# Kernel optimization log

Measured on AMD Instinct MI355X. Metric: run time of the kernel, lower is better.

The kernel has to match this reference:

```python
import jax, jax.numpy as jnp
import numpy as np

INNER_LR = 0.001
INNER_STEPS = 3
EPS = 1e-8


def setup_inputs() -> dict:
    key = jax.random.key(0)
    ks = jax.random.split(key, 9)
    B_, H, K = 16384, 512, 64
    return {
        "R_U": jax.random.normal(ks[0], (B_, H, 3), dtype=jnp.float32),
        "alpha": jax.random.uniform(ks[1], (B_,), dtype=jnp.float32),
        "beta": jax.random.uniform(ks[2], (B_,), dtype=jnp.float32),
        "lambdas": jax.random.uniform(ks[3], (3,), dtype=jnp.float32),
        "B": jax.random.normal(ks[4], (H, K), dtype=jnp.float32),
        "B_dot": jax.random.normal(ks[5], (H, K), dtype=jnp.float32),
        "B_ddot": jax.random.normal(ks[6], (H, K), dtype=jnp.float32),
        "B_dddot": jax.random.normal(ks[7], (H, K), dtype=jnp.float32),
        "B_pinv": jax.random.normal(ks[8], (K, H), dtype=jnp.float32),
    }


def _inner_opt(R_U, alpha, beta, lambdas, B, B_dot, B_ddot, B_dddot, B_pinv):
    l1, l2, l3 = lambdas[0], lambdas[1], lambdas[2]

    def per_sample(r, a, b):
        # r: (H,3); C: (K,3)
        C0 = B_pinv @ r

        def loss_fn(C):
            P = B @ C            # (H,3)
            V = B_dot @ C        # (H,3)
            A = B_ddot @ C       # (H,3)
            J = B_dddot @ C      # (H,3)
            v_norm_raw = jnp.linalg.norm(V, axis=-1)          # (H,) used in power-law loss
            v_norm_eps = v_norm_raw + EPS                      # used in curvature (torch adds eps)
            cross = jnp.cross(V, A)                            # (H,3)
            kappa = jnp.linalg.norm(cross, axis=-1) / (v_norm_eps ** 3 + EPS)
            pos_loss = jnp.sum((P - r) ** 2, axis=-1)          # (H,)
            kappa_safe = jnp.clip(kappa, 1e-4, 1e4)
            log_power = jnp.clip(b * jnp.log(kappa_safe), -10.0, 10.0)
            target = jnp.clip(a * jnp.exp(log_power), 1e-6, 1e6)
            power_law_loss = (v_norm_raw - target) ** 2        # (H,)
            jerk_loss = jnp.sum(J ** 2, axis=-1)               # (H,)
            return jnp.sum(l1 * pos_loss + l2 * power_law_loss + l3 * jerk_loss)

        def step(C, _):
            g = jax.grad(loss_fn)(C)
            return C - INNER_LR * g, None

        C, _ = jax.lax.scan(step, C0, None, length=INNER_STEPS)
        return C

    return jax.vmap(per_sample)(R_U, alpha, beta)  # (batch, K, 3)


def reference(R_U, alpha, beta, lambdas, B, B_dot, B_ddot, B_dddot, B_pinv):
    return _inner_opt(R_U, alpha, beta, lambdas, B, B_dot, B_ddot, B_dddot, B_pinv)
```

## Files before the change

kernel.cpp:

```cpp
#include <hip/hip_runtime.h>
#include <hip/hip_bf16.h>
#include <math.h>

#define EPSF 1e-8f
#define LR   1e-3f

#define HH 512
#define KK 64
#define SS 8
#define PbStr 104
#define GbStr 136
#define SLICE 4096

typedef short    bf16x8 __attribute__((ext_vector_type(8)));
typedef _Float16 f16x8  __attribute__((ext_vector_type(8)));
typedef _Float16 f16x4  __attribute__((ext_vector_type(4)));
typedef float    f32x4  __attribute__((ext_vector_type(4)));

__device__ __forceinline__ unsigned short f2bf(float x) {
  unsigned int u = __float_as_uint(x);
  return (unsigned short)((u + 0x7fffu + ((u >> 16) & 1u)) >> 16);
}
__device__ __forceinline__ float bfhi(float x) {
  return __uint_as_float(((unsigned int)f2bf(x)) << 16);
}
__device__ __forceinline__ unsigned short f2h(float x) {
  _Float16 h = (_Float16)x;
  return *(unsigned short*)&h;
}
__device__ __forceinline__ unsigned int pkbf2(float a, float b) {
  union { __hip_bfloat162 h; unsigned int u; } cv;
  cv.h = __float22bfloat162_rn(make_float2(a, b));
  return cv.u;
}

__device__ __forceinline__ void elemf(
    float P0, float P1, float P2, float V0, float V1, float V2,
    float A0, float A1, float A2, float J0, float J1, float J2,
    float aa, float bb, float r0, float r1, float r2,
    float l1, float l2, float l3,
    float& o0, float& o1, float& o2, float& o3, float& o4, float& o5,
    float& o6, float& o7, float& o8, float& o9, float& o10, float& o11) {
  float v2 = V0*V0 + V1*V1 + V2*V2;
  float v  = __builtin_amdgcn_sqrtf(v2);
  float ve = v + EPSF;
  float cx0 = V1*A2 - V2*A1;
  float cx1 = V2*A0 - V0*A2;
  float cx2 = V0*A1 - V1*A0;
  float nc  = __builtin_amdgcn_sqrtf(cx0*cx0 + cx1*cx1 + cx2*cx2);
  float ve2 = ve*ve;
  float denom = ve2*ve + EPSF;
  float invd  = __builtin_amdgcn_rcpf(denom);
  float kappa = nc * invd;
  float ks  = fminf(fmaxf(kappa, 1e-4f), 1e4f);
  float lpr = bb * __logf(ks);
  float lp  = fminf(fmaxf(lpr, -10.f), 10.f);
  float tr  = aa * __expf(lp);
  float tt  = fminf(fmaxf(tr, 1e-6f), 1e6f);
  float s2  = 2.f*l2*(v - tt);
  float gtr  = (tr > 1e-6f && tr < 1e6f) ? -s2 : 0.f;
  float glpr = (lpr > -10.f && lpr < 10.f) ? gtr*tr : 0.f;
  float gk   = (kappa > 1e-4f && kappa < 1e4f)
                 ? glpr*bb*__builtin_amdgcn_rcpf(ks) : 0.f;
  float gnc  = gk * invd;
  float gden = -gk * kappa * invd;
  float gve  = 3.f * ve2 * gden;
  float gv   = s2 + gve;
  float giv  = gv * __builtin_amdgcn_rcpf(v);
  float gcs  = gnc * __builtin_amdgcn_rcpf(nc);
  float gc0 = gcs*cx0, gc1 = gcs*cx1, gc2 = gcs*cx2;
  o0  = 2.f*l1*(P0 - r0);
  o1  = 2.f*l1*(P1 - r1);
  o2  = 2.f*l1*(P2 - r2);
  o3  = fmaf(giv, V0, A1*gc2 - A2*gc1);
  o4  = fmaf(giv, V1, A2*gc0 - A0*gc2);
  o5  = fmaf(giv, V2, A0*gc1 - A1*gc0);
  o6  = gc1*V2 - gc2*V1;
  o7  = gc2*V0 - gc0*V2;
  o8  = gc0*V1 - gc1*V0;
  o9  = 2.f*l3*J0;
  o10 = 2.f*l3*J1;
  o11 = 2.f*l3*J2;
}

__global__ void prep_kernel(const float* __restrict__ B,
                            const float* __restrict__ Bd,
                            const float* __restrict__ Bdd,
                            const float* __restrict__ Bddd,
                            const float* __restrict__ Bp,
                            unsigned short* __restrict__ ws) {
  int tid = blockIdx.x * 256 + threadIdx.x;
  const float* Ms[4] = {B, Bd, Bdd, Bddd};
  unsigned short bits[2];
  if (tid < 65536) {
    #pragma unroll
    for (int t = 0; t < 2; ++t) {
      unsigned int id = 2u * tid + t;
      int j = id & 7, lane = (id >> 3) & 63;
      int mt = (id >> 9) & 3, ks2 = (id >> 11) & 3;
      int qtr = (id >> 13) & 3, chunk = (id >> 15) & 3;
      int khat = mt * 16 + (lane & 15);
      int kq = ((lane >> 4) << 3) + j;
      int h = chunk * 128 + qtr * 32 + kq;
      bits[t] = f2bf(Ms[ks2][h * 64 + khat]);
    }
    ((unsigned int*)ws)[tid] = ((unsigned int)bits[1] << 16) | bits[0];
  } else if (tid < 131072) {
    int base = tid - 65536;
    #pragma unroll
    for (int t = 0; t < 2; ++t) {
      unsigned int id = 2u * base + t;
      int j = id & 7, lane = (id >> 3) & 63, kap = (id >> 9) & 1;
      int ht = (id >> 10) & 31, z = (id >> 15) & 3;
      int h = ht * 16 + (lane & 15);
      int kk = kap * 32 + ((lane >> 4) << 3) + j;
      bits[t] = f2h(Ms[z][h * 64 + kk]);
    }
    ((unsigned int*)(ws + 131072))[base] = ((unsigned int)bits[1] << 16) | bits[0];
  } else {
    int base = tid - 131072;
    #pragma unroll
    for (int t = 0; t < 2; ++t) {
      unsigned int id = 2u * base + t;
      int j = id & 7, lane = (id >> 3) & 63, hilo = (id >> 9) & 1;
      int mt = (id >> 10) & 3, ks = (id >> 12) & 15;
      int khat = mt * 16 + (lane & 15);
      int Kl = ks * 32 + ((lane >> 4) << 3) + j;
      float val = Bp[khat * 512 + Kl];
      float hi = bfhi(val);
      bits[t] = hilo ? f2bf(val - hi) : f2bf(hi);
    }
    ((unsigned int*)(ws + 262144))[base] = ((unsigned int)bits[1] << 16) | bits[0];
  }
}

__global__ __launch_bounds__(256, 3)
void copt_kernel(const float* __restrict__ R_U,
                 const float* __restrict__ alpha,
                 const float* __restrict__ beta,
                 const float* __restrict__ lambdas,
                 const unsigned short* __restrict__ ws,
                 float* __restrict__ out) {
  __shared__ __align__(16) float Cl[SS][KK][3];
  __shared__ __align__(16) unsigned short Cbf[2 * 1024];
  __shared__ __align__(16) unsigned short pool[4 * SLICE];

  const unsigned short* AFb = ws;
  const unsigned short* AFf = ws + 131072;
  const unsigned short* AFp = ws + 262144;

  const int tid  = threadIdx.x;
  const int lane = tid & 63;
  const int wid  = tid >> 6;
  const int quad = lane >> 4;
  const int c    = lane & 15;

  const float l1 = lambdas[0], l2 = lambdas[1], l3 = lambdas[2];
  const int bg = blockIdx.x * SS;

  ((float4*)Cbf)[tid] = make_float4(0.f, 0.f, 0.f, 0.f);

  #pragma unroll
  for (int sg2 = 0; sg2 < 2; ++sg2) {
    const int colb = sg2 * 12 + 3 * wid;
    const float4* rp = (const float4*)(R_U + (size_t)(bg + wid + sg2 * 4) * (HH * 3));
    #pragma unroll
    for (int i = 0; i < 6; ++i) {
      float4 v = rp[i * 64 + lane];
      int e = (i * 64 + lane) * 4;
      const float* pv = &v.x;
      #pragma unroll
      for (int d = 0; d < 4; ++d) {
        int ee = e + d, h = ee / 3, m = ee - 3 * h;
        pool[(colb + m) * 520 + h] = f2bf(pv[d]);
      }
    }
  }
  __syncthreads();

  {
    f32x4 cacc0 = {0.f, 0.f, 0.f, 0.f};
    f32x4 cacc1 = {0.f, 0.f, 0.f, 0.f};
    const unsigned short* gb0 = &pool[c * 520 + quad * 8];
    const unsigned short* gb1 = &pool[(12 + c) * 520 + quad * 8];
    #pragma unroll 4
    for (int ks = 0; ks < 16; ++ks) {
      const unsigned short* pA = AFp + (size_t)((ks * 4 + wid) * 2) * 512 + lane * 8;
      bf16x8 ah = *(const bf16x8*)pA;
      bf16x8 al = *(const bf16x8*)(pA + 512);
      bf16x8 g0 = *(const bf16x8*)(gb0 + ks * 32);
      bf16x8 g1 = *(const bf16x8*)(gb1 + ks * 32);
      cacc0 = __builtin_amdgcn_mfma_f32_16x16x32_bf16(ah, g0, cacc0, 0, 0, 0);
      cacc0 = __builtin_amdgcn_mfma_f32_16x16x32_bf16(al, g0, cacc0, 0, 0, 0);
      cacc1 = __builtin_amdgcn_mfma_f32_16x16x32_bf16(ah, g1, cacc1, 0, 0, 0);
      cacc1 = __builtin_amdgcn_mfma_f32_16x16x32_bf16(al, g1, cacc1, 0, 0, 0);
    }
    if (c < 12) {
      const int sl = (c * 86) >> 8, m = c - 3 * sl;
      const int kr = wid * 16 + quad * 4;
      #pragma unroll
      for (int r = 0; r < 4; ++r) {
        int k = kr + r;
        float v0 = cacc0[r];
        Cl[sl][k][m] = v0;
        Cbf[(k >> 5) * 512 + (((k >> 3) & 3) * 16 + c) * 8 + (k & 7)] = f2h(v0);
        float v1 = cacc1[r];
        Cl[sl + 4][k][m] = v1;
        Cbf[1024 + (k >> 5) * 512 + (((k >> 3) & 3) * 16 + c) * 8 + (k & 7)] = f2h(v1);
      }
    }
  }
  __syncthreads();

  const int hq = lane & 31;
  const int esb = 4 * (lane >> 5);
  const float ea0 = alpha[bg + esb + 0], ea1 = alpha[bg + esb + 1];
  const float ea2 = alpha[bg + esb + 2], ea3 = alpha[bg + esb + 3];
  const float eb0 = beta[bg + esb + 0],  eb1 = beta[bg + esb + 1];
  const float eb2 = beta[bg + esb + 2],  eb3 = beta[bg + esb + 3];
  const float* er0 = R_U + (size_t)(bg + esb + 0) * (HH * 3);
  const float* er1 = R_U + (size_t)(bg + esb + 1) * (HH * 3);
  const float* er2 = R_U + (size_t)(bg + esb + 2) * (HH * 3);
  const float* er3 = R_U + (size_t)(bg + esb + 3) * (HH * 3);

  unsigned short* Pbh = pool + wid * SLICE;
  unsigned short* Gbu = pool + wid * SLICE;

  const int fs = (c * 86) >> 8, fm = c - 3 * fs;

  for (int it = 0; it < 3; ++it) {
    f32x4 g00 = {0.f,0.f,0.f,0.f}, g01 = {0.f,0.f,0.f,0.f};
    f32x4 g10 = {0.f,0.f,0.f,0.f}, g11 = {0.f,0.f,0.f,0.f};
    f32x4 g20 = {0.f,0.f,0.f,0.f}, g21 = {0.f,0.f,0.f,0.f};
    f32x4 g30 = {0.f,0.f,0.f,0.f}, g31 = {0.f,0.f,0.f,0.f};

    f16x8 cf00 = *(const f16x8*)&Cbf[lane * 8];
    f16x8 cf01 = *(const f16x8*)&Cbf[512 + lane * 8];
    f16x8 cf10 = *(const f16x8*)&Cbf[1024 + lane * 8];
    f16x8 cf11 = *(const f16x8*)&Cbf[1536 + lane * 8];

    for (int q = 0; q < 4; ++q) {
      #pragma unroll
      for (int ht = 0; ht < 2; ++ht) {
        const int htg = wid * 8 + q * 2 + ht;
        #pragma unroll
        for (int z = 0; z < 4; ++z) {
          const unsigned short* pA =
              AFf + (size_t)((z * 32 + htg) * 2) * 512 + lane * 8;
          f16x8 af0 = *(const f16x8*)pA;
          f16x8 af1 = *(const f16x8*)(pA + 512);
          f32x4 d0 = {0.f, 0.f, 0.f, 0.f};
          d0 = __builtin_amdgcn_mfma_f32_16x16x32_f16(af0, cf00, d0, 0, 0, 0);
          d0 = __builtin_amdgcn_mfma_f32_16x16x32_f16(af1, cf01, d0, 0, 0, 0);
          f32x4 d1 = {0.f, 0.f, 0.f, 0.f};
          d1 = __builtin_amdgcn_mfma_f32_16x16x32_f16(af0, cf10, d1, 0, 0, 0);
          d1 = __builtin_amdgcn_mfma_f32_16x16x32_f16(af1, cf11, d1, 0, 0, 0);
          if (c < 12) {
            unsigned short* pb = Pbh + (ht * 16 + quad * 4) * PbStr + z * 3 + fm;
            unsigned short* pp0 = pb + fs * 12;
            pp0[0 * PbStr] = f2h(d0[0]);
            pp0[1 * PbStr] = f2h(d0[1]);
            pp0[2 * PbStr] = f2h(d0[2]);
            pp0[3 * PbStr] = f2h(d0[3]);
            unsigned short* pp1 = pb + (fs + 4) * 12;
            pp1[0 * PbStr] = f2h(d1[0]);
            pp1[1 * PbStr] = f2h(d1[1]);
            pp1[2 * PbStr] = f2h(d1[2]);
            pp1[3 * PbStr] = f2h(d1[3]);
          }
        }
      }

      {
        const unsigned short* p0 = Pbh + hq * PbStr + (esb + 0) * 12;
        const unsigned short* p1 = Pbh + hq * PbStr + (esb + 1) * 12;
        const unsigned short* p2 = Pbh + hq * PbStr + (esb + 2) * 12;
        const unsigned short* p3 = Pbh + hq * PbStr + (esb + 3) * 12;
        f16x4 va0 = *(const f16x4*)(p0);
        f16x4 va1 = *(const f16x4*)(p0 + 4);
        f16x4 va2 = *(const f16x4*)(p0 + 8);
        f16x4 vb0 = *(const f16x4*)(p1);
        f16x4 vb1 = *(const f16x4*)(p1 + 4);
        f16x4 vb2 = *(const f16x4*)(p1 + 8);
        f16x4 vc0 = *(const f16x4*)(p2);
        f16x4 vc1 = *(const f16x4*)(p2 + 4);
        f16x4 vc2 = *(const f16x4*)(p2 + 8);
        f16x4 vd0 = *(const f16x4*)(p3);
        f16x4 vd1 = *(const f16x4*)(p3 + 4);
        f16x4 vd2 = *(const f16x4*)(p3 + 8);
        const int hg = wid * 128 + q * 32 + hq;
        float r00 = er0[(size_t)hg*3], r01 = er0[(size_t)hg*3+1], r02 = er0[(size_t)hg*3+2];
        float r10 = er1[(size_t)hg*3], r11 = er1[(size_t)hg*3+1], r12 = er1[(size_t)hg*3+2];
        float r20 = er2[(size_t)hg*3], r21 = er2[(size_t)hg*3+1], r22 = er2[(size_t)hg*3+2];
        float r30 = er3[(size_t)hg*3], r31 = er3[(size_t)hg*3+1], r32 = er3[(size_t)hg*3+2];

        float gA0,gA1,gA2,gA3,gA4,gA5,gA6,gA7,gA8,gA9,gA10,gA11;
        float gB0,gB1,gB2,gB3,gB4,gB5,gB6,gB7,gB8,gB9,gB10,gB11;
        elemf((float)va0[0],(float)va0[1],(float)va0[2],(float)va0[3],
              (float)va1[0],(float)va1[1],(float)va1[2],(float)va1[3],
              (float)va2[0],(float)va2[1],(float)va2[2],(float)va2[3],
              ea0, eb0, r00, r01, r02, l1, l2, l3,
              gA0,gA1,gA2,gA3,gA4,gA5,gA6,gA7,gA8,gA9,gA10,gA11);
        elemf((float)vb0[0],(float)vb0[1],(float)vb0[2],(float)vb0[3],
              (float)vb1[0],(float)vb1[1],(float)vb1[2],(float)vb1[3],
              (float)vb2[0],(float)vb2[1],(float)vb2[2],(float)vb2[3],
              ea1, eb1, r10, r11, r12, l1, l2, l3,
              gB0,gB1,gB2,gB3,gB4,gB5,gB6,gB7,gB8,gB9,gB10,gB11);

        #define STOREG(zz, mm, GA, GB, E0, E1) { \
          unsigned int pk = pkbf2(GA, GB); \
          Gbu[(3*(esb+E0) + mm) * GbStr + (zz)*32 + hq] = (unsigned short)pk; \
          Gbu[(3*(esb+E1) + mm) * GbStr + (zz)*32 + hq] = (unsigned short)(pk >> 16); }
        STOREG(0, 0, gA0, gB0, 0, 1)  STOREG(0, 1, gA1, gB1, 0, 1)  STOREG(0, 2, gA2, gB2, 0, 1)
        STOREG(1, 0, gA3, gB3, 0, 1)  STOREG(1, 1, gA4, gB4, 0, 1)  STOREG(1, 2, gA5, gB5, 0, 1)
        STOREG(2, 0, gA6, gB6, 0, 1)  STOREG(2, 1, gA7, gB7, 0, 1)  STOREG(2, 2, gA8, gB8, 0, 1)
        STOREG(3, 0, gA9, gB9, 0, 1)  STOREG(3, 1, gA10, gB10, 0, 1) STOREG(3, 2, gA11, gB11, 0, 1)

        elemf((float)vc0[0],(float)vc0[1],(float)vc0[2],(float)vc0[3],
              (float)vc1[0],(float)vc1[1],(float)vc1[2],(float)vc1[3],
              (float)vc2[0],(float)vc2[1],(float)vc2[2],(float)vc2[3],
              ea2, eb2, r20, r21, r22, l1, l2, l3,
              gA0,gA1,gA2,gA3,gA4,gA5,gA6,gA7,gA8,gA9,gA10,gA11);
        elemf((float)vd0[0],(float)vd0[1],(float)vd0[2],(float)vd0[3],
              (float)vd1[0],(float)vd1[1],(float)vd1[2],(float)vd1[3],
              (float)vd2[0],(float)vd2[1],(float)vd2[2],(float)vd2[3],
              ea3, eb3, r30, r31, r32, l1, l2, l3,
              gB0,gB1,gB2,gB3,gB4,gB5,gB6,gB7,gB8,gB9,gB10,gB11);
        STOREG(0, 0, gA0, gB0, 2, 3)  STOREG(0, 1, gA1, gB1, 2, 3)  STOREG(0, 2, gA2, gB2, 2, 3)
        STOREG(1, 0, gA3, gB3, 2, 3)  STOREG(1, 1, gA4, gB4, 2, 3)  STOREG(1, 2, gA5, gB5, 2, 3)
        STOREG(2, 0, gA6, gB6, 2, 3)  STOREG(2, 1, gA7, gB7, 2, 3)  STOREG(2, 2, gA8, gB8, 2, 3)
        STOREG(3, 0, gA9, gB9, 2, 3)  STOREG(3, 1, gA10, gB10, 2, 3) STOREG(3, 2, gA11, gB11, 2, 3)
        #undef STOREG
      }

      #pragma unroll
      for (int ks2 = 0; ks2 < 4; ++ks2) {
        bf16x8 gg0 = *(const bf16x8*)&Gbu[c * GbStr + ks2 * 32 + quad * 8];
        bf16x8 gg1 = *(const bf16x8*)&Gbu[(12 + c) * GbStr + ks2 * 32 + quad * 8];
        const unsigned short* pA0 =
            AFb + (size_t)(((wid * 4 + q) * 4 + ks2) * 4) * 512 + lane * 8;
        bf16x8 a0 = *(const bf16x8*)(pA0);
        bf16x8 a1 = *(const bf16x8*)(pA0 + 512);
        bf16x8 a2 = *(const bf16x8*)(pA0 + 1024);
        bf16x8 a3 = *(const bf16x8*)(pA0 + 1536);
        g00 = __builtin_amdgcn_mfma_f32_16x16x32_bf16(a0, gg0, g00, 0, 0, 0);
        g01 = __builtin_amdgcn_mfma_f32_16x16x32_bf16(a0, gg1, g01, 0, 0, 0);
        g10 = __builtin_amdgcn_mfma_f32_16x16x32_bf16(a1, gg0, g10, 0, 0, 0);
        g11 = __builtin_amdgcn_mfma_f32_16x16x32_bf16(a1, gg1, g11, 0, 0, 0);
        g20 = __builtin_amdgcn_mfma_f32_16x16x32_bf16(a2, gg0, g20, 0, 0, 0);
        g21 = __builtin_amdgcn_mfma_f32_16x16x32_bf16(a2, gg1, g21, 0, 0, 0);
        g30 = __builtin_amdgcn_mfma_f32_16x16x32_bf16(a3, gg0, g30, 0, 0, 0);
        g31 = __builtin_amdgcn_mfma_f32_16x16x32_bf16(a3, gg1, g31, 0, 0, 0);
      }
    }

    {
      float* dmp = (float*)pool + wid * (SLICE / 2);
      *(f32x4*)(dmp +    0 + lane * 4) = g00;
      *(f32x4*)(dmp +  256 + lane * 4) = g01;
      *(f32x4*)(dmp +  512 + lane * 4) = g10;
      *(f32x4*)(dmp +  768 + lane * 4) = g11;
      *(f32x4*)(dmp + 1024 + lane * 4) = g20;
      *(f32x4*)(dmp + 1280 + lane * 4) = g21;
      *(f32x4*)(dmp + 1536 + lane * 4) = g30;
      *(f32x4*)(dmp + 1792 + lane * 4) = g31;
    }
    __syncthreads();
    {
      const float* poolF = (const float*)pool;
      f32x4 tot0 = {0.f, 0.f, 0.f, 0.f};
      f32x4 tot1 = {0.f, 0.f, 0.f, 0.f};
      #pragma unroll
      for (int v = 0; v < 4; ++v) {
        tot0 += *(const f32x4*)(poolF + v * (SLICE / 2) + (wid * 2 + 0) * 256 + lane * 4);
        tot1 += *(const f32x4*)(poolF + v * (SLICE / 2) + (wid * 2 + 1) * 256 + lane * 4);
      }
      if (c < 12) {
        const int sl = (c * 86) >> 8, m = c - 3 * sl;
        const int kr = wid * 16 + quad * 4;
        #pragma unroll
        for (int r = 0; r < 4; ++r) {
          int k = kr + r;
          float v0 = Cl[sl][k][m] - LR * tot0[r];
          Cl[sl][k][m] = v0;
          Cbf[(k >> 5) * 512 + (((k >> 3) & 3) * 16 + c) * 8 + (k & 7)] = f2h(v0);
          float v1 = Cl[sl + 4][k][m] - LR * tot1[r];
          Cl[sl + 4][k][m] = v1;
          Cbf[1024 + (k >> 5) * 512 + (((k >> 3) & 3) * 16 + c) * 8 + (k & 7)] = f2h(v1);
        }
      }
    }
    __syncthreads();
  }

  #pragma unroll
  for (int sg2 = 0; sg2 < 2; ++sg2) {
    const int ps = wid + sg2 * 4;
    float* op = out + ((size_t)(bg + ps) * KK + lane) * 3;
    op[0] = Cl[ps][lane][0];
    op[1] = Cl[ps][lane][1];
    op[2] = Cl[ps][lane][2];
  }
}

extern "C" void kernel_launch(void* const* d_in, const int* in_sizes, int n_in,
                              void* d_out, int out_size, void* d_ws, size_t ws_size,
                              hipStream_t stream) {
  const float* R_U     = (const float*)d_in[0];
  const float* alpha   = (const float*)d_in[1];
  const float* beta    = (const float*)d_in[2];
  const float* lambdas = (const float*)d_in[3];
  const float* B       = (const float*)d_in[4];
  const float* Bd      = (const float*)d_in[5];
  const float* Bdd     = (const float*)d_in[6];
  const float* Bddd    = (const float*)d_in[7];
  const float* Bp      = (const float*)d_in[8];
  unsigned short* ws = (unsigned short*)d_ws;
  const int nB = in_sizes[1];

  hipLaunchKernelGGL(prep_kernel, dim3(640), dim3(256), 0, stream,
                     B, Bd, Bdd, Bddd, Bp, ws);
  hipLaunchKernelGGL(copt_kernel, dim3(nB / SS), dim3(256), 0, stream,
                     R_U, alpha, beta, lambdas, ws, (float*)d_out);
}
```

Measured before the change: 369.0 us.

## Keep C coefficients in registers, drop Cl LDS array, raise occupancy to four blocks

```diff
diff --git a/kernel.cpp b/kernel.cpp
--- a/kernel.cpp
+++ b/kernel.cpp
@@ -8,9 +8,10 @@
 #define HH 512
 #define KK 64
 #define SS 8
-#define PbStr 104
+#define PbStr 100
 #define GbStr 136
 #define SLICE 4096
+#define OutStr 193
 
 typedef short    bf16x8 __attribute__((ext_vector_type(8)));
 typedef _Float16 f16x8  __attribute__((ext_vector_type(8)));
@@ -134,14 +135,13 @@
   }
 }
 
-__global__ __launch_bounds__(256, 3)
+__global__ __launch_bounds__(256, 4)
 void copt_kernel(const float* __restrict__ R_U,
                  const float* __restrict__ alpha,
                  const float* __restrict__ beta,
                  const float* __restrict__ lambdas,
                  const unsigned short* __restrict__ ws,
                  float* __restrict__ out) {
-  __shared__ __align__(16) float Cl[SS][KK][3];
   __shared__ __align__(16) unsigned short Cbf[2 * 1024];
   __shared__ __align__(16) unsigned short pool[4 * SLICE];
 
@@ -178,9 +178,12 @@
   }
   __syncthreads();
 
+  f32x4 Creg0 = {0.f, 0.f, 0.f, 0.f};
+  f32x4 Creg1 = {0.f, 0.f, 0.f, 0.f};
+  const int sl = (c * 86) >> 8, fm = c - 3 * sl;
+  const int kr = wid * 16 + quad * 4;
+
   {
-    f32x4 cacc0 = {0.f, 0.f, 0.f, 0.f};
-    f32x4 cacc1 = {0.f, 0.f, 0.f, 0.f};
     const unsigned short* gb0 = &pool[c * 520 + quad * 8];
     const unsigned short* gb1 = &pool[(12 + c) * 520 + quad * 8];
     #pragma unroll 4
@@ -190,23 +193,17 @@
       bf16x8 al = *(const bf16x8*)(pA + 512);
       bf16x8 g0 = *(const bf16x8*)(gb0 + ks * 32);
       bf16x8 g1 = *(const bf16x8*)(gb1 + ks * 32);
-      cacc0 = __builtin_amdgcn_mfma_f32_16x16x32_bf16(ah, g0, cacc0, 0, 0, 0);
-      cacc0 = __builtin_amdgcn_mfma_f32_16x16x32_bf16(al, g0, cacc0, 0, 0, 0);
-      cacc1 = __builtin_amdgcn_mfma_f32_16x16x32_bf16(ah, g1, cacc1, 0, 0, 0);
-      cacc1 = __builtin_amdgcn_mfma_f32_16x16x32_bf16(al, g1, cacc1, 0, 0, 0);
+      Creg0 = __builtin_amdgcn_mfma_f32_16x16x32_bf16(ah, g0, Creg0, 0, 0, 0);
+      Creg0 = __builtin_amdgcn_mfma_f32_16x16x32_bf16(al, g0, Creg0, 0, 0, 0);
+      Creg1 = __builtin_amdgcn_mfma_f32_16x16x32_bf16(ah, g1, Creg1, 0, 0, 0);
+      Creg1 = __builtin_amdgcn_mfma_f32_16x16x32_bf16(al, g1, Creg1, 0, 0, 0);
     }
     if (c < 12) {
-      const int sl = (c * 86) >> 8, m = c - 3 * sl;
-      const int kr = wid * 16 + quad * 4;
       #pragma unroll
       for (int r = 0; r < 4; ++r) {
         int k = kr + r;
-        float v0 = cacc0[r];
-        Cl[sl][k][m] = v0;
-        Cbf[(k >> 5) * 512 + (((k >> 3) & 3) * 16 + c) * 8 + (k & 7)] = f2h(v0);
-        float v1 = cacc1[r];
-        Cl[sl + 4][k][m] = v1;
-        Cbf[1024 + (k >> 5) * 512 + (((k >> 3) & 3) * 16 + c) * 8 + (k & 7)] = f2h(v1);
+        Cbf[(k >> 5) * 512 + (((k >> 3) & 3) * 16 + c) * 8 + (k & 7)] = f2h(Creg0[r]);
+        Cbf[1024 + (k >> 5) * 512 + (((k >> 3) & 3) * 16 + c) * 8 + (k & 7)] = f2h(Creg1[r]);
       }
     }
   }
@@ -225,8 +222,6 @@
 
   unsigned short* Pbh = pool + wid * SLICE;
   unsigned short* Gbu = pool + wid * SLICE;
-
-  const int fs = (c * 86) >> 8, fm = c - 3 * fs;
 
   for (int it = 0; it < 3; ++it) {
     f32x4 g00 = {0.f,0.f,0.f,0.f}, g01 = {0.f,0.f,0.f,0.f};
@@ -257,12 +252,12 @@
           d1 = __builtin_amdgcn_mfma_f32_16x16x32_f16(af1, cf11, d1, 0, 0, 0);
           if (c < 12) {
             unsigned short* pb = Pbh + (ht * 16 + quad * 4) * PbStr + z * 3 + fm;
-            unsigned short* pp0 = pb + fs * 12;
+            unsigned short* pp0 = pb + sl * 12;
             pp0[0 * PbStr] = f2h(d0[0]);
             pp0[1 * PbStr] = f2h(d0[1]);
             pp0[2 * PbStr] = f2h(d0[2]);
             pp0[3 * PbStr] = f2h(d0[3]);
-            unsigned short* pp1 = pb + (fs + 4) * 12;
+            unsigned short* pp1 = pb + (sl + 4) * 12;
             pp1[0 * PbStr] = f2h(d1[0]);
             pp1[1 * PbStr] = f2h(d1[1]);
             pp1[2 * PbStr] = f2h(d1[2]);
@@ -375,31 +370,42 @@
         tot0 += *(const f32x4*)(poolF + v * (SLICE / 2) + (wid * 2 + 0) * 256 + lane * 4);
         tot1 += *(const f32x4*)(poolF + v * (SLICE / 2) + (wid * 2 + 1) * 256 + lane * 4);
       }
-      if (c < 12) {
-        const int sl = (c * 86) >> 8, m = c - 3 * sl;
-        const int kr = wid * 16 + quad * 4;
+      Creg0 -= LR * tot0;
+      Creg1 -= LR * tot1;
+      if (c < 12 && it < 2) {
         #pragma unroll
         for (int r = 0; r < 4; ++r) {
           int k = kr + r;
-          float v0 = Cl[sl][k][m] - LR * tot0[r];
-          Cl[sl][k][m] = v0;
-          Cbf[(k >> 5) * 512 + (((k >> 3) & 3) * 16 + c) * 8 + (k & 7)] = f2h(v0);
-          float v1 = Cl[sl + 4][k][m] - LR * tot1[r];
-          Cl[sl + 4][k][m] = v1;
-          Cbf[1024 + (k >> 5) * 512 + (((k >> 3) & 3) * 16 + c) * 8 + (k & 7)] = f2h(v1);
+          Cbf[(k >> 5) * 512 + (((k >> 3) & 3) * 16 + c) * 8 + (k & 7)] = f2h(Creg0[r]);
+          Cbf[1024 + (k >> 5) * 512 + (((k >> 3) & 3) * 16 + c) * 8 + (k & 7)] = f2h(Creg1[r]);
         }
       }
     }
     __syncthreads();
   }
 
-  #pragma unroll
-  for (int sg2 = 0; sg2 < 2; ++sg2) {
-    const int ps = wid + sg2 * 4;
-    float* op = out + ((size_t)(bg + ps) * KK + lane) * 3;
-    op[0] = Cl[ps][lane][0];
-    op[1] = Cl[ps][lane][1];
-    op[2] = Cl[ps][lane][2];
+  {
+    float* poolF = (float*)pool;
+    if (c < 12) {
+      #pragma unroll
+      for (int r = 0; r < 4; ++r) {
+        int k = kr + r;
+        poolF[sl * OutStr + k * 3 + fm]       = Creg0[r];
+        poolF[(sl + 4) * OutStr + k * 3 + fm] = Creg1[r];
+      }
+    }
+  }
+  __syncthreads();
+  {
+    const float* poolF = (const float*)pool;
+    #pragma unroll
+    for (int sg2 = 0; sg2 < 2; ++sg2) {
+      const int ps = wid + sg2 * 4;
+      float* op = out + ((size_t)(bg + ps) * KK + lane) * 3;
+      op[0] = poolF[ps * OutStr + lane * 3 + 0];
+      op[1] = poolF[ps * OutStr + lane * 3 + 1];
+      op[2] = poolF[ps * OutStr + lane * 3 + 2];
+    }
   }
 }
 
```

New measurement: 452.3 us. 1.23x slower.
